# Optimization experiments

Measured on AMD Instinct MI355X. Metric: run time of the kernel, lower is better.

## Reference

```python
import jax, jax.numpy as jnp
import numpy as np

N_NODES = 100000
N_EDGES = 800000
IN_DIM, HID_DIM, OUT_DIM = 256, 128, 64


def setup_inputs() -> dict:
    key = jax.random.key(0)
    k1, k2, k3, k4 = jax.random.split(key, 4)
    x = jax.random.normal(k1, (N_NODES, IN_DIM), dtype=jnp.float32)
    edge_index = jax.random.randint(k2, (2, N_EDGES), 0, N_NODES, dtype=jnp.int64)
    # Glorot-style init scaled params
    W1 = jax.random.normal(k3, (IN_DIM, HID_DIM), dtype=jnp.float32) * (1.0 / np.sqrt(IN_DIM))
    b1 = jnp.zeros((HID_DIM,), dtype=jnp.float32)
    W2 = jax.random.normal(k4, (HID_DIM, OUT_DIM), dtype=jnp.float32) * (1.0 / np.sqrt(HID_DIM))
    b2 = jnp.zeros((OUT_DIM,), dtype=jnp.float32)
    return {"x": x, "edge_index": edge_index, "W1": W1, "b1": b1, "W2": W2, "b2": b2}


def reference(x, edge_index, W1, b1, W2, b2):
    n = x.shape[0]
    # GCNConv default: add self-loops, symmetric normalization D^-1/2 (A+I) D^-1/2
    loop = jnp.arange(n, dtype=edge_index.dtype)
    src = jnp.concatenate([edge_index[0], loop])
    dst = jnp.concatenate([edge_index[1], loop])
    deg = jax.ops.segment_sum(jnp.ones(src.shape, dtype=x.dtype), dst, num_segments=n)
    dinv = jax.lax.rsqrt(deg)  # deg >= 1 thanks to self-loops
    norm = dinv[src] * dinv[dst]  # [E+N]

    def gcn_conv(h, W, b):
        hw = h @ W                                         # [N, d_out] dense transform first (d_out < d_in)
        msg = hw[src] * norm[:, None]                      # gather + scale, [E+N, d_out]
        agg = jax.ops.segment_sum(msg, dst, num_segments=n)
        return agg + b

    h = jax.nn.relu(gcn_conv(x, W1, b1))
    return gcn_conv(h, W2, b2)
```

## Files before the change

### kernel.cpp

```cpp
#include <hip/hip_runtime.h>

typedef unsigned int uint;
typedef unsigned short ushort;
typedef __attribute__((ext_vector_type(8))) short bf16x8;
typedef __attribute__((ext_vector_type(4))) float f32x4;

#define NN 100000
#define NE 800000
#define D_IN 256
#define D_HID 128
#define D_OUT 64

__device__ __forceinline__ ushort f2bf(float f) {
    uint u = __float_as_uint(f);
    return (ushort)((u + 0x7fffu + ((u >> 16) & 1u)) >> 16);
}
__device__ __forceinline__ float bflo(uint u) { return __uint_as_float(u << 16); }
__device__ __forceinline__ float bfhi(uint u) { return __uint_as_float(u & 0xffff0000u); }

__global__ __launch_bounds__(256) void k_count(const int* __restrict__ dst, int* __restrict__ count, int e) {
    int i = blockIdx.x * 256 + threadIdx.x;
    if (i < e) {
        unsigned d = (unsigned)dst[i];
        if (d < NN) atomicAdd(&count[d], 1);
    }
}

#define SCAN_B 1024
__global__ __launch_bounds__(SCAN_B) void k_scan1(const int* __restrict__ count, int* __restrict__ incl,
                                                  int* __restrict__ blocksum, int n) {
    __shared__ int tmp[SCAN_B];
    int t = threadIdx.x;
    int gid = blockIdx.x * SCAN_B + t;
    int v = (gid < n) ? count[gid] : 0;
    tmp[t] = v;
    __syncthreads();
    for (int off = 1; off < SCAN_B; off <<= 1) {
        int u = (t >= off) ? tmp[t - off] : 0;
        __syncthreads();
        tmp[t] += u;
        __syncthreads();
    }
    if (gid < n) incl[gid] = tmp[t];
    if (t == SCAN_B - 1) blocksum[blockIdx.x] = tmp[t];
}

__global__ __launch_bounds__(128) void k_scan2(const int* __restrict__ blocksum, int* __restrict__ blockoff, int nb) {
    __shared__ int tmp[128];
    int t = threadIdx.x;
    int v = (t < nb) ? blocksum[t] : 0;
    tmp[t] = v;
    __syncthreads();
    for (int off = 1; off < 128; off <<= 1) {
        int u = (t >= off) ? tmp[t - off] : 0;
        __syncthreads();
        tmp[t] += u;
        __syncthreads();
    }
    blockoff[t] = tmp[t] - v;
}

__global__ __launch_bounds__(256) void k_scan3(const int* __restrict__ incl, const int* __restrict__ count,
                                               const int* __restrict__ blockoff, int* __restrict__ offsets,
                                               int* __restrict__ cursor, float* __restrict__ dinv, int n) {
    int i = blockIdx.x * 256 + threadIdx.x;
    if (i < n) {
        int inc = incl[i] + blockoff[i >> 10];
        int exc = inc - count[i];
        offsets[i] = exc;
        cursor[i] = exc;
        dinv[i] = rsqrtf((float)(count[i] + 1));
        if (i == n - 1) offsets[n] = inc;
    }
}

__global__ __launch_bounds__(256) void k_scatter(const int* __restrict__ edges, int* __restrict__ cursor,
                                                 int* __restrict__ srcs, int e) {
    int i = blockIdx.x * 256 + threadIdx.x;
    if (i < e) {
        unsigned s = (unsigned)edges[i];
        unsigned d = (unsigned)edges[e + i];
        if (s < NN && d < NN) {
            int pos = atomicAdd(&cursor[d], 1);
            srcs[pos] = (int)s;
        }
    }
}

__global__ __launch_bounds__(256) void k_cast4(const float* __restrict__ in, ushort* __restrict__ out, int n4) {
    int i = blockIdx.x * 256 + threadIdx.x;
    if (i < n4) {
        const float4 v = *reinterpret_cast<const float4*>(in + (size_t)i * 4);
        uint2 o;
        o.x = (uint)f2bf(v.x) | ((uint)f2bf(v.y) << 16);
        o.y = (uint)f2bf(v.z) | ((uint)f2bf(v.w) << 16);
        *reinterpret_cast<uint2*>(out + (size_t)i * 4) = o;
    }
}

__global__ __launch_bounds__(256) void k_castT(const float* __restrict__ W, ushort* __restrict__ WT, int K, int N) {
    int t = blockIdx.x * 256 + threadIdx.x;
    if (t < K * N) {
        int n = t / K, k = t % K;
        WT[t] = f2bf(W[(size_t)k * N + n]);
    }
}

template <int K_DIM, int N_DIM>
__global__ __launch_bounds__(256) void k_gemm_mfma(const ushort* __restrict__ A, const ushort* __restrict__ BT,
                                                   const float* __restrict__ dinv, ushort* __restrict__ C, int M) {
    constexpr int NF = N_DIM / 16;
    constexpr int KK = K_DIM / 32;
    const int tid = threadIdx.x;
    const int w = tid >> 6, lane = tid & 63;
    const int l15 = lane & 15, g = lane >> 4;
    const int row0 = blockIdx.x * 128 + w * 32;

    f32x4 acc[2][NF];
#pragma unroll
    for (int mf = 0; mf < 2; mf++)
#pragma unroll
        for (int nf = 0; nf < NF; nf++) acc[mf][nf] = (f32x4){0.f, 0.f, 0.f, 0.f};

    const int rA0 = min(row0 + l15, M - 1);
    const int rA1 = min(row0 + 16 + l15, M - 1);
    const ushort* pa0 = A + (size_t)rA0 * K_DIM + g * 8;
    const ushort* pa1 = A + (size_t)rA1 * K_DIM + g * 8;
    const ushort* pb = BT + (size_t)l15 * K_DIM + g * 8;

#pragma unroll
    for (int kk = 0; kk < KK; ++kk) {
        bf16x8 a0 = *reinterpret_cast<const bf16x8*>(pa0 + kk * 32);
        bf16x8 a1 = *reinterpret_cast<const bf16x8*>(pa1 + kk * 32);
#pragma unroll
        for (int nf = 0; nf < NF; nf++) {
            bf16x8 b = *reinterpret_cast<const bf16x8*>(pb + (size_t)nf * 16 * K_DIM + kk * 32);
            acc[0][nf] = __builtin_amdgcn_mfma_f32_16x16x32_bf16(a0, b, acc[0][nf], 0, 0, 0);
            acc[1][nf] = __builtin_amdgcn_mfma_f32_16x16x32_bf16(a1, b, acc[1][nf], 0, 0, 0);
        }
    }

#pragma unroll
    for (int mf = 0; mf < 2; mf++) {
#pragma unroll
        for (int r = 0; r < 4; r++) {
            int row = row0 + mf * 16 + g * 4 + r;
            if (row < M) {
                float dv = dinv[row];
#pragma unroll
                for (int nf = 0; nf < NF; nf++)
                    C[(size_t)row * N_DIM + nf * 16 + l15] = f2bf(acc[mf][nf][r] * dv);
            }
        }
    }
}

__global__ __launch_bounds__(256) void k_agg128(const ushort* __restrict__ hws, const int* __restrict__ srcs,
                                                const int* __restrict__ offs, const float* __restrict__ dinv,
                                                const float* __restrict__ bias, ushort* __restrict__ outb, int n) {
    const int wv = threadIdx.x >> 6, lane = threadIdx.x & 63;
    const int node = blockIdx.x * 4 + wv;
    if (node >= n) return;
    const int beg = offs[node], end = offs[node + 1];
    const uint* base = (const uint*)hws;
    uint us = base[(size_t)node * 64 + lane];
    float a0 = bflo(us), a1 = bfhi(us);
    int e = beg;
    for (; e + 1 < end; e += 2) {
        int s0 = srcs[e], s1 = srcs[e + 1];
        uint u0 = base[(size_t)s0 * 64 + lane];
        uint u1 = base[(size_t)s1 * 64 + lane];
        a0 += bflo(u0); a1 += bfhi(u0);
        a0 += bflo(u1); a1 += bfhi(u1);
    }
    if (e < end) {
        uint u0 = base[(size_t)srcs[e] * 64 + lane];
        a0 += bflo(u0); a1 += bfhi(u0);
    }
    const float dv = dinv[node];
    float v0 = fmaxf(a0 * dv + bias[lane * 2], 0.f);
    float v1 = fmaxf(a1 * dv + bias[lane * 2 + 1], 0.f);
    ((uint*)outb)[(size_t)node * 64 + lane] = (uint)f2bf(v0) | ((uint)f2bf(v1) << 16);
}

__global__ __launch_bounds__(256) void k_agg64(const ushort* __restrict__ hws, const int* __restrict__ srcs,
                                               const int* __restrict__ offs, const float* __restrict__ dinv,
                                               const float* __restrict__ bias, float* __restrict__ out, int n) {
    const int wv = threadIdx.x >> 6, lane = threadIdx.x & 63;
    const int node = blockIdx.x * 4 + wv;
    if (node >= n) return;
    const int beg = offs[node], end = offs[node + 1];
    float a = bflo((uint)hws[(size_t)node * 64 + lane]);
    int e = beg;
    for (; e + 1 < end; e += 2) {
        int s0 = srcs[e], s1 = srcs[e + 1];
        float f0 = bflo((uint)hws[(size_t)s0 * 64 + lane]);
        float f1 = bflo((uint)hws[(size_t)s1 * 64 + lane]);
        a += f0 + f1;
    }
    if (e < end) a += bflo((uint)hws[(size_t)srcs[e] * 64 + lane]);
    out[(size_t)node * 64 + lane] = a * dinv[node] + bias[lane];
}

static inline size_t align_up(size_t x, size_t a) { return (x + a - 1) & ~(a - 1); }

extern "C" void kernel_launch(void* const* d_in, const int* in_sizes, int n_in,
                              void* d_out, int out_size, void* d_ws, size_t ws_size,
                              hipStream_t stream) {
    const float* x = (const float*)d_in[0];
    const int* edges = (const int*)d_in[1];
    const float* W1 = (const float*)d_in[2];
    const float* b1 = (const float*)d_in[3];
    const float* W2 = (const float*)d_in[4];
    const float* b2 = (const float*)d_in[5];
    float* out = (float*)d_out;

    char* p = (char*)d_ws;
    int* count = (int*)p;     p += align_up(NN * 4, 256);
    int* incl = (int*)p;      p += align_up(NN * 4, 256);
    int* offsets = (int*)p;   p += align_up((NN + 1) * 4, 256);
    int* cursor = (int*)p;    p += align_up(NN * 4, 256);
    int* srcs = (int*)p;      p += align_up(NE * 4, 256);
    int* blocksum = (int*)p;  p += align_up(256 * 4, 256);
    int* blockoff = (int*)p;  p += align_up(256 * 4, 256);
    float* dinv = (float*)p;  p += align_up(NN * 4, 256);
    ushort* w1t = (ushort*)p; p += align_up(D_IN * D_HID * 2, 256);
    ushort* w2t = (ushort*)p; p += align_up(D_HID * D_OUT * 2, 256);
    ushort* xb = (ushort*)p;  p += align_up((size_t)NN * D_IN * 2, 256);
    ushort* hw1s = (ushort*)p; p += align_up((size_t)NN * D_HID * 2, 256);
    ushort* hb = (ushort*)p;   p += align_up((size_t)NN * D_HID * 2, 256);
    ushort* hw2s = xb;

    const int nb_scan = (NN + SCAN_B - 1) / SCAN_B;

    hipMemsetAsync(count, 0, NN * 4, stream);
    k_count<<<(NE + 255) / 256, 256, 0, stream>>>(edges + NE, count, NE);
    k_scan1<<<nb_scan, SCAN_B, 0, stream>>>(count, incl, blocksum, NN);
    k_scan2<<<1, 128, 0, stream>>>(blocksum, blockoff, nb_scan);
    k_scan3<<<(NN + 255) / 256, 256, 0, stream>>>(incl, count, blockoff, offsets, cursor, dinv, NN);
    k_scatter<<<(NE + 255) / 256, 256, 0, stream>>>(edges, cursor, srcs, NE);

    k_cast4<<<(NN * D_IN / 4 + 255) / 256, 256, 0, stream>>>(x, xb, NN * D_IN / 4);
    k_castT<<<(D_IN * D_HID + 255) / 256, 256, 0, stream>>>(W1, w1t, D_IN, D_HID);
    k_castT<<<(D_HID * D_OUT + 255) / 256, 256, 0, stream>>>(W2, w2t, D_HID, D_OUT);

    const int gemm_blocks = (NN + 127) / 128;

    k_gemm_mfma<D_IN, D_HID><<<gemm_blocks, 256, 0, stream>>>(xb, w1t, dinv, hw1s, NN);
    k_agg128<<<(NN + 3) / 4, 256, 0, stream>>>(hw1s, srcs, offsets, dinv, b1, hb, NN);

    k_gemm_mfma<D_HID, D_OUT><<<gemm_blocks, 256, 0, stream>>>(hb, w2t, dinv, hw2s, NN);
    k_agg64<<<(NN + 3) / 4, 256, 0, stream>>>(hw2s, srcs, offsets, dinv, b2, out, NN);
}
```

Baseline: 433.9 us.

## Fuse input cast into GEMM, merge scan and weight-cast kernels, vectorize aggregation

The first GEMM now reads fp32 x directly and converts to bf16 in registers, which removes the separate cast kernel and its 51 MB write plus re-read. The scan2 kernel is folded into scan3, where each thread sums the block totals serially from shared memory, and the two weight-cast kernels are merged into one. The aggregation kernels now give each lane 16-byte loads and split each node's neighbours across lane groups, combining partial sums with cross-lane shuffles. The cost is a per-thread serial loop of up to about 98 iterations in scan3 and shuffle-reduction overhead in aggregation.

```diff
diff --git a/kernel.cpp b/kernel.cpp
--- a/kernel.cpp
+++ b/kernel.cpp
@@ -17,6 +17,15 @@
 }
 __device__ __forceinline__ float bflo(uint u) { return __uint_as_float(u << 16); }
 __device__ __forceinline__ float bfhi(uint u) { return __uint_as_float(u & 0xffff0000u); }
+__device__ __forceinline__ uint pack2(float lo, float hi) {
+    return (uint)f2bf(lo) | ((uint)f2bf(hi) << 16);
+}
+__device__ __forceinline__ bf16x8 pack8(float4 a, float4 b) {
+    bf16x8 r;
+    r[0] = (short)f2bf(a.x); r[1] = (short)f2bf(a.y); r[2] = (short)f2bf(a.z); r[3] = (short)f2bf(a.w);
+    r[4] = (short)f2bf(b.x); r[5] = (short)f2bf(b.y); r[6] = (short)f2bf(b.z); r[7] = (short)f2bf(b.w);
+    return r;
+}
 
 __global__ __launch_bounds__(256) void k_count(const int* __restrict__ dst, int* __restrict__ count, int e) {
     int i = blockIdx.x * 256 + threadIdx.x;
@@ -45,27 +54,19 @@
     if (t == SCAN_B - 1) blocksum[blockIdx.x] = tmp[t];
 }
 
-__global__ __launch_bounds__(128) void k_scan2(const int* __restrict__ blocksum, int* __restrict__ blockoff, int nb) {
-    __shared__ int tmp[128];
+__global__ __launch_bounds__(256) void k_scan3(const int* __restrict__ incl, const int* __restrict__ count,
+                                               const int* __restrict__ blocksum, int nb, int* __restrict__ offsets,
+                                               int* __restrict__ cursor, float* __restrict__ dinv, int n) {
+    __shared__ int bs[128];
     int t = threadIdx.x;
-    int v = (t < nb) ? blocksum[t] : 0;
-    tmp[t] = v;
+    if (t < 128) bs[t] = (t < nb) ? blocksum[t] : 0;
     __syncthreads();
-    for (int off = 1; off < 128; off <<= 1) {
-        int u = (t >= off) ? tmp[t - off] : 0;
-        __syncthreads();
-        tmp[t] += u;
-        __syncthreads();
-    }
-    blockoff[t] = tmp[t] - v;
-}
-
-__global__ __launch_bounds__(256) void k_scan3(const int* __restrict__ incl, const int* __restrict__ count,
-                                               const int* __restrict__ blockoff, int* __restrict__ offsets,
-                                               int* __restrict__ cursor, float* __restrict__ dinv, int n) {
-    int i = blockIdx.x * 256 + threadIdx.x;
+    int i = blockIdx.x * 256 + t;
     if (i < n) {
-        int inc = incl[i] + blockoff[i >> 10];
+        int b = i >> 10;
+        int off = 0;
+        for (int j = 0; j < b; j++) off += bs[j];
+        int inc = incl[i] + off;
         int exc = inc - count[i];
         offsets[i] = exc;
         cursor[i] = exc;
@@ -87,27 +88,23 @@
     }
 }
 
-__global__ __launch_bounds__(256) void k_cast4(const float* __restrict__ in, ushort* __restrict__ out, int n4) {
-    int i = blockIdx.x * 256 + threadIdx.x;
-    if (i < n4) {
-        const float4 v = *reinterpret_cast<const float4*>(in + (size_t)i * 4);
-        uint2 o;
-        o.x = (uint)f2bf(v.x) | ((uint)f2bf(v.y) << 16);
-        o.y = (uint)f2bf(v.z) | ((uint)f2bf(v.w) << 16);
-        *reinterpret_cast<uint2*>(out + (size_t)i * 4) = o;
-    }
-}
-
-__global__ __launch_bounds__(256) void k_castT(const float* __restrict__ W, ushort* __restrict__ WT, int K, int N) {
+__global__ __launch_bounds__(256) void k_castW(const float* __restrict__ W1, const float* __restrict__ W2,
+                                               ushort* __restrict__ w1t, ushort* __restrict__ w2t) {
     int t = blockIdx.x * 256 + threadIdx.x;
-    if (t < K * N) {
-        int n = t / K, k = t % K;
-        WT[t] = f2bf(W[(size_t)k * N + n]);
-    }
-}
-
-template <int K_DIM, int N_DIM>
-__global__ __launch_bounds__(256) void k_gemm_mfma(const ushort* __restrict__ A, const ushort* __restrict__ BT,
+    if (t < D_IN * D_HID) {
+        int n = t / D_IN, k = t % D_IN;
+        w1t[t] = f2bf(W1[(size_t)k * D_HID + n]);
+    } else {
+        int u = t - D_IN * D_HID;
+        if (u < D_HID * D_OUT) {
+            int n = u / D_HID, k = u % D_HID;
+            w2t[u] = f2bf(W2[(size_t)k * D_OUT + n]);
+        }
+    }
+}
+
+template <int K_DIM, int N_DIM, bool AF32>
+__global__ __launch_bounds__(256) void k_gemm_mfma(const void* __restrict__ Av, const ushort* __restrict__ BT,
                                                    const float* __restrict__ dinv, ushort* __restrict__ C, int M) {
     constexpr int NF = N_DIM / 16;
     constexpr int KK = K_DIM / 32;
@@ -124,14 +121,22 @@
 
     const int rA0 = min(row0 + l15, M - 1);
     const int rA1 = min(row0 + 16 + l15, M - 1);
-    const ushort* pa0 = A + (size_t)rA0 * K_DIM + g * 8;
-    const ushort* pa1 = A + (size_t)rA1 * K_DIM + g * 8;
     const ushort* pb = BT + (size_t)l15 * K_DIM + g * 8;
 
 #pragma unroll
     for (int kk = 0; kk < KK; ++kk) {
-        bf16x8 a0 = *reinterpret_cast<const bf16x8*>(pa0 + kk * 32);
-        bf16x8 a1 = *reinterpret_cast<const bf16x8*>(pa1 + kk * 32);
+        bf16x8 a0, a1;
+        if constexpr (AF32) {
+            const float* A = (const float*)Av;
+            const float4* p0 = (const float4*)(A + (size_t)rA0 * K_DIM + g * 8 + kk * 32);
+            const float4* p1 = (const float4*)(A + (size_t)rA1 * K_DIM + g * 8 + kk * 32);
+            a0 = pack8(p0[0], p0[1]);
+            a1 = pack8(p1[0], p1[1]);
+        } else {
+            const ushort* A = (const ushort*)Av;
+            a0 = *reinterpret_cast<const bf16x8*>(A + (size_t)rA0 * K_DIM + g * 8 + kk * 32);
+            a1 = *reinterpret_cast<const bf16x8*>(A + (size_t)rA1 * K_DIM + g * 8 + kk * 32);
+        }
 #pragma unroll
         for (int nf = 0; nf < NF; nf++) {
             bf16x8 b = *reinterpret_cast<const bf16x8*>(pb + (size_t)nf * 16 * K_DIM + kk * 32);
@@ -161,26 +166,46 @@
     const int wv = threadIdx.x >> 6, lane = threadIdx.x & 63;
     const int node = blockIdx.x * 4 + wv;
     if (node >= n) return;
-    const int beg = offs[node], end = offs[node + 1];
-    const uint* base = (const uint*)hws;
-    uint us = base[(size_t)node * 64 + lane];
-    float a0 = bflo(us), a1 = bfhi(us);
-    int e = beg;
-    for (; e + 1 < end; e += 2) {
-        int s0 = srcs[e], s1 = srcs[e + 1];
-        uint u0 = base[(size_t)s0 * 64 + lane];
-        uint u1 = base[(size_t)s1 * 64 + lane];
-        a0 += bflo(u0); a1 += bfhi(u0);
-        a0 += bflo(u1); a1 += bfhi(u1);
-    }
-    if (e < end) {
-        uint u0 = base[(size_t)srcs[e] * 64 + lane];
-        a0 += bflo(u0); a1 += bfhi(u0);
-    }
-    const float dv = dinv[node];
-    float v0 = fmaxf(a0 * dv + bias[lane * 2], 0.f);
-    float v1 = fmaxf(a1 * dv + bias[lane * 2 + 1], 0.f);
-    ((uint*)outb)[(size_t)node * 64 + lane] = (uint)f2bf(v0) | ((uint)f2bf(v1) << 16);
+    const int g = lane >> 4, l15 = lane & 15;
+    const int beg = offs[node];
+    const int T = offs[node + 1] - beg + 1;
+    const uint4* base = (const uint4*)hws;
+    float acc[8] = {};
+    int t = g;
+    for (; t + 4 < T; t += 8) {
+        int s0 = (t == 0) ? node : srcs[beg + t - 1];
+        int s1 = srcs[beg + t + 3];
+        uint4 va = base[(size_t)s0 * 16 + l15];
+        uint4 vb = base[(size_t)s1 * 16 + l15];
+        acc[0] += bflo(va.x) + bflo(vb.x); acc[1] += bfhi(va.x) + bfhi(vb.x);
+        acc[2] += bflo(va.y) + bflo(vb.y); acc[3] += bfhi(va.y) + bfhi(vb.y);
+        acc[4] += bflo(va.z) + bflo(vb.z); acc[5] += bfhi(va.z) + bfhi(vb.z);
+        acc[6] += bflo(va.w) + bflo(vb.w); acc[7] += bfhi(va.w) + bfhi(vb.w);
+    }
+    for (; t < T; t += 4) {
+        int s0 = (t == 0) ? node : srcs[beg + t - 1];
+        uint4 va = base[(size_t)s0 * 16 + l15];
+        acc[0] += bflo(va.x); acc[1] += bfhi(va.x);
+        acc[2] += bflo(va.y); acc[3] += bfhi(va.y);
+        acc[4] += bflo(va.z); acc[5] += bfhi(va.z);
+        acc[6] += bflo(va.w); acc[7] += bfhi(va.w);
+    }
+#pragma unroll
+    for (int j = 0; j < 8; j++) {
+        acc[j] += __shfl_xor(acc[j], 16);
+        acc[j] += __shfl_xor(acc[j], 32);
+    }
+    if (g == 0) {
+        const float dv = dinv[node];
+        const float4* b4 = (const float4*)(bias + 8 * l15);
+        float4 bb0 = b4[0], bb1 = b4[1];
+        uint4 o;
+        o.x = pack2(fmaxf(acc[0] * dv + bb0.x, 0.f), fmaxf(acc[1] * dv + bb0.y, 0.f));
+        o.y = pack2(fmaxf(acc[2] * dv + bb0.z, 0.f), fmaxf(acc[3] * dv + bb0.w, 0.f));
+        o.z = pack2(fmaxf(acc[4] * dv + bb1.x, 0.f), fmaxf(acc[5] * dv + bb1.y, 0.f));
+        o.w = pack2(fmaxf(acc[6] * dv + bb1.z, 0.f), fmaxf(acc[7] * dv + bb1.w, 0.f));
+        ((uint4*)outb)[(size_t)node * 16 + l15] = o;
+    }
 }
 
 __global__ __launch_bounds__(256) void k_agg64(const ushort* __restrict__ hws, const int* __restrict__ srcs,
@@ -189,17 +214,48 @@
     const int wv = threadIdx.x >> 6, lane = threadIdx.x & 63;
     const int node = blockIdx.x * 4 + wv;
     if (node >= n) return;
-    const int beg = offs[node], end = offs[node + 1];
-    float a = bflo((uint)hws[(size_t)node * 64 + lane]);
-    int e = beg;
-    for (; e + 1 < end; e += 2) {
-        int s0 = srcs[e], s1 = srcs[e + 1];
-        float f0 = bflo((uint)hws[(size_t)s0 * 64 + lane]);
-        float f1 = bflo((uint)hws[(size_t)s1 * 64 + lane]);
-        a += f0 + f1;
-    }
-    if (e < end) a += bflo((uint)hws[(size_t)srcs[e] * 64 + lane]);
-    out[(size_t)node * 64 + lane] = a * dinv[node] + bias[lane];
+    const int g = lane >> 3, l7 = lane & 7;
+    const int beg = offs[node];
+    const int T = offs[node + 1] - beg + 1;
+    const uint4* base = (const uint4*)hws;
+    float acc[8] = {};
+    int t = g;
+    for (; t + 8 < T; t += 16) {
+        int s0 = (t == 0) ? node : srcs[beg + t - 1];
+        int s1 = srcs[beg + t + 7];
+        uint4 va = base[(size_t)s0 * 8 + l7];
+        uint4 vb = base[(size_t)s1 * 8 + l7];
+        acc[0] += bflo(va.x) + bflo(vb.x); acc[1] += bfhi(va.x) + bfhi(vb.x);
+        acc[2] += bflo(va.y) + bflo(vb.y); acc[3] += bfhi(va.y) + bfhi(vb.y);
+        acc[4] += bflo(va.z) + bflo(vb.z); acc[5] += bfhi(va.z) + bfhi(vb.z);
+        acc[6] += bflo(va.w) + bflo(vb.w); acc[7] += bfhi(va.w) + bfhi(vb.w);
+    }
+    for (; t < T; t += 8) {
+        int s0 = (t == 0) ? node : srcs[beg + t - 1];
+        uint4 va = base[(size_t)s0 * 8 + l7];
+        acc[0] += bflo(va.x); acc[1] += bfhi(va.x);
+        acc[2] += bflo(va.y); acc[3] += bfhi(va.y);
+        acc[4] += bflo(va.z); acc[5] += bfhi(va.z);
+        acc[6] += bflo(va.w); acc[7] += bfhi(va.w);
+    }
+#pragma unroll
+    for (int j = 0; j < 8; j++) {
+        acc[j] += __shfl_xor(acc[j], 8);
+        acc[j] += __shfl_xor(acc[j], 16);
+        acc[j] += __shfl_xor(acc[j], 32);
+    }
+    if (g == 0) {
+        const float dv = dinv[node];
+        const float4* b4 = (const float4*)(bias + 8 * l7);
+        float4 bb0 = b4[0], bb1 = b4[1];
+        float4 o0, o1;
+        o0.x = acc[0] * dv + bb0.x; o0.y = acc[1] * dv + bb0.y;
+        o0.z = acc[2] * dv + bb0.z; o0.w = acc[3] * dv + bb0.w;
+        o1.x = acc[4] * dv + bb1.x; o1.y = acc[5] * dv + bb1.y;
+        o1.z = acc[6] * dv + bb1.z; o1.w = acc[7] * dv + bb1.w;
+        ((float4*)out)[(size_t)node * 16 + 2 * l7] = o0;
+        ((float4*)out)[(size_t)node * 16 + 2 * l7 + 1] = o1;
+    }
 }
 
 static inline size_t align_up(size_t x, size_t a) { return (x + a - 1) & ~(a - 1); }
@@ -216,39 +272,33 @@
     float* out = (float*)d_out;
 
     char* p = (char*)d_ws;
-    int* count = (int*)p;     p += align_up(NN * 4, 256);
-    int* incl = (int*)p;      p += align_up(NN * 4, 256);
-    int* offsets = (int*)p;   p += align_up((NN + 1) * 4, 256);
-    int* cursor = (int*)p;    p += align_up(NN * 4, 256);
-    int* srcs = (int*)p;      p += align_up(NE * 4, 256);
-    int* blocksum = (int*)p;  p += align_up(256 * 4, 256);
-    int* blockoff = (int*)p;  p += align_up(256 * 4, 256);
-    float* dinv = (float*)p;  p += align_up(NN * 4, 256);
-    ushort* w1t = (ushort*)p; p += align_up(D_IN * D_HID * 2, 256);
-    ushort* w2t = (ushort*)p; p += align_up(D_HID * D_OUT * 2, 256);
-    ushort* xb = (ushort*)p;  p += align_up((size_t)NN * D_IN * 2, 256);
+    int* count = (int*)p;      p += align_up(NN * 4, 256);
+    int* incl = (int*)p;       p += align_up(NN * 4, 256);
+    int* offsets = (int*)p;    p += align_up((NN + 1) * 4, 256);
+    int* cursor = (int*)p;     p += align_up(NN * 4, 256);
+    int* srcs = (int*)p;       p += align_up(NE * 4, 256);
+    int* blocksum = (int*)p;   p += align_up(256 * 4, 256);
+    float* dinv = (float*)p;   p += align_up(NN * 4, 256);
+    ushort* w1t = (ushort*)p;  p += align_up(D_IN * D_HID * 2, 256);
+    ushort* w2t = (ushort*)p;  p += align_up(D_HID * D_OUT * 2, 256);
     ushort* hw1s = (ushort*)p; p += align_up((size_t)NN * D_HID * 2, 256);
     ushort* hb = (ushort*)p;   p += align_up((size_t)NN * D_HID * 2, 256);
-    ushort* hw2s = xb;
+    ushort* hw2s = (ushort*)p; p += align_up((size_t)NN * D_OUT * 2, 256);
 
     const int nb_scan = (NN + SCAN_B - 1) / SCAN_B;
 
     hipMemsetAsync(count, 0, NN * 4, stream);
     k_count<<<(NE + 255) / 256, 256, 0, stream>>>(edges + NE, count, NE);
     k_scan1<<<nb_scan, SCAN_B, 0, stream>>>(count, incl, blocksum, NN);
-    k_scan2<<<1, 128, 0, stream>>>(blocksum, blockoff, nb_scan);
-    k_scan3<<<(NN + 255) / 256, 256, 0, stream>>>(incl, count, blockoff, offsets, cursor, dinv, NN);
+    k_scan3<<<(NN + 255) / 256, 256, 0, stream>>>(incl, count, blocksum, nb_scan, offsets, cursor, dinv, NN);
     k_scatter<<<(NE + 255) / 256, 256, 0, stream>>>(edges, cursor, srcs, NE);
-
-    k_cast4<<<(NN * D_IN / 4 + 255) / 256, 256, 0, stream>>>(x, xb, NN * D_IN / 4);
-    k_castT<<<(D_IN * D_HID + 255) / 256, 256, 0, stream>>>(W1, w1t, D_IN, D_HID);
-    k_castT<<<(D_HID * D_OUT + 255) / 256, 256, 0, stream>>>(W2, w2t, D_HID, D_OUT);
+    k_castW<<<(D_IN * D_HID + D_HID * D_OUT + 255) / 256, 256, 0, stream>>>(W1, W2, w1t, w2t);
 
     const int gemm_blocks = (NN + 127) / 128;
 
-    k_gemm_mfma<D_IN, D_HID><<<gemm_blocks, 256, 0, stream>>>(xb, w1t, dinv, hw1s, NN);
+    k_gemm_mfma<D_IN, D_HID, true><<<gemm_blocks, 256, 0, stream>>>(x, w1t, dinv, hw1s, NN);
     k_agg128<<<(NN + 3) / 4, 256, 0, stream>>>(hw1s, srcs, offsets, dinv, b1, hb, NN);
 
-    k_gemm_mfma<D_HID, D_OUT><<<gemm_blocks, 256, 0, stream>>>(hb, w2t, dinv, hw2s, NN);
+    k_gemm_mfma<D_HID, D_OUT, false><<<gemm_blocks, 256, 0, stream>>>(hb, w2t, dinv, hw2s, NN);
     k_agg64<<<(NN + 3) / 4, 256, 0, stream>>>(hw2s, srcs, offsets, dinv, b2, out, NN);
 }
```

Result: faster. 392.2 us (-9.6%).
